# Optimization experiments

Hardware: AMD Instinct MI355X
Metric: run time of the kernel (lower is better)

Reference implementation:

```python
import math
import jax, jax.numpy as jnp
import numpy as np

B, N, TOKEN_DIM = 8, 8192, 512
NODE_DIM = 64
MAX_NODES = 64
SCORE_HIDDEN = 64


def setup_inputs() -> dict:
    key = jax.random.key(0)
    ks = jax.random.split(key, 8)
    s = lambda k, shape, fan_in: jax.random.normal(k, shape, jnp.float32) / np.sqrt(fan_in)
    return {
        "token_feats": jax.random.normal(ks[0], (B, N, TOKEN_DIM), jnp.float32),
        "score_w1": s(ks[1], (TOKEN_DIM, SCORE_HIDDEN), TOKEN_DIM),
        "score_b1": jnp.zeros((SCORE_HIDDEN,), jnp.float32),
        "score_w2": s(ks[2], (SCORE_HIDDEN, 1), SCORE_HIDDEN),
        "score_b2": jnp.zeros((1,), jnp.float32),
        "t2n_w": s(ks[3], (TOKEN_DIM, NODE_DIM), TOKEN_DIM),
        "n2t_w": s(ks[4], (NODE_DIM, TOKEN_DIM), NODE_DIM),
        "gcn_w1": s(ks[5], (NODE_DIM, NODE_DIM), NODE_DIM),
        "gcn_w2": s(ks[6], (NODE_DIM, NODE_DIM), NODE_DIM),
    }


def reference(token_feats, score_w1, score_b1, score_w2, score_b2,
              t2n_w, n2t_w, gcn_w1, gcn_w2):
    Bn, Nn, d = token_feats.shape
    M = MAX_NODES
    eps = 1e-6

    # --- node selection (scores -> threshold -> top-k among selected) ---
    h = jax.nn.relu(jnp.einsum('bnd,dh->bnh', token_feats, score_w1) + score_b1)
    scores = (jnp.einsum('bnh,ho->bno', h, score_w2) + score_b2)[..., 0]  # [B,N]
    mean = scores.mean(axis=1, keepdims=True)
    std = scores.std(axis=1, keepdims=True)  # unbiased=False (population)
    thr = mean + 0.5 * std
    count = jnp.sum(scores > thr, axis=1)  # [B]
    fallback_k = min(M, max(4, Nn // 16))
    take_k = jnp.where(count == 0, fallback_k, jnp.minimum(count, M))  # [B]

    _, top_idx = jax.lax.top_k(scores, M)  # [B,M] highest scores; set == torch's selection
    node_mask = jnp.arange(M)[None, :] < take_k[:, None]  # [B,M] bool
    maskf = node_mask.astype(token_feats.dtype)

    gathered = jnp.take_along_axis(token_feats, top_idx[..., None], axis=1)  # [B,M,d]
    H0 = jnp.einsum('bmd,dk->bmk', gathered, t2n_w) * maskf[..., None]  # [B,M,node_dim]

    # --- cosine-similarity adjacency, masked, self-loops, row-normalized ---
    nrm = jnp.maximum(jnp.linalg.norm(H0, axis=-1, keepdims=True), eps)
    Hn = H0 / nrm
    A = jax.nn.relu(jnp.einsum('bik,bjk->bij', Hn, Hn))
    A = A * (maskf[:, :, None] * maskf[:, None, :])
    A = A + jnp.eye(M, dtype=A.dtype)[None] * maskf[:, None, :]
    A = A / jnp.maximum(A.sum(axis=-1, keepdims=True), 1e-6)

    # --- two-layer GCN (no bias) ---
    x = jax.nn.relu(jnp.einsum('bij,bjk,kl->bil', A, H0, gcn_w1))
    Hg = jax.nn.relu(jnp.einsum('bij,bjk,kl->bil', A, x, gcn_w2))  # [B,M,node_dim]

    # --- attention scatter-back to tokens ---
    token_proj = jnp.einsum('bnd,dk->bnk', token_feats, t2n_w)  # [B,N,node_dim]
    logits = jnp.einsum('bnk,bmk->bnm', token_proj, Hg) / math.sqrt(NODE_DIM)
    attn = jax.nn.softmax(logits, axis=-1)
    injected = jnp.einsum('bnm,bmk->bnk', attn, Hg)
    back = jnp.einsum('bnk,kd->bnd', injected, n2t_w)
    return token_feats + back
```

## Files before the change

### kernel.cpp

```cpp
#include <hip/hip_runtime.h>
#include <hip/hip_bf16.h>

#define B_ 8
#define N_ 8192
#define D_ 512
#define M_ 64

typedef unsigned short u16;
typedef unsigned int u32;
typedef __attribute__((ext_vector_type(8))) short bf16x8;
typedef __attribute__((ext_vector_type(4))) float f32x4;

__device__ __forceinline__ u16 f2bf(float f) {
  u32 u = __float_as_uint(f);
  u += 0x7FFFu + ((u >> 16) & 1u);
  return (u16)(u >> 16);
}
__device__ __forceinline__ float bf2f(u16 h) {
  return __uint_as_float(((u32)h) << 16);
}

__device__ __forceinline__ int bfrag_idx(int kd, int c, int ncols16) {
  int sub = (kd >> 5) * ncols16 + (c >> 4);
  int lane = (c & 15) + 16 * ((kd & 15) >> 2);
  int e = (kd & 3) + 4 * ((kd >> 4) & 1);
  return sub * 512 + lane * 8 + e;
}

__device__ __forceinline__ int kslot(int ln, int e) {
  return (e & 3) + 4 * (ln >> 4) + 16 * (e >> 2);
}

__device__ __forceinline__ bf16x8 pack8(float4 v0, float4 v1) {
  bf16x8 a;
  a[0] = (short)f2bf(v0.x); a[1] = (short)f2bf(v0.y);
  a[2] = (short)f2bf(v0.z); a[3] = (short)f2bf(v0.w);
  a[4] = (short)f2bf(v1.x); a[5] = (short)f2bf(v1.y);
  a[6] = (short)f2bf(v1.z); a[7] = (short)f2bf(v1.w);
  return a;
}

__global__ __launch_bounds__(256) void k_prep(
    const float* __restrict__ t2n, const float* __restrict__ n2t,
    const float* __restrict__ W1, const float* __restrict__ g1,
    const float* __restrict__ g2,
    u16* __restrict__ t2nf, u16* __restrict__ n2tf,
    u16* __restrict__ W1h, u16* __restrict__ W1l,
    u16* __restrict__ g1f, u16* __restrict__ g2f)
{
  const int gid = blockIdx.x * 256 + threadIdx.x;
  const int stride = gridDim.x * 256;
  for (int s = gid; s < 512 * 64; s += stride) {
    const int k = s >> 6, c = s & 63;
    const int idx = bfrag_idx(k, c, 4);
    t2nf[idx] = f2bf(t2n[s]);
    const float w = W1[s];
    const u16 wh = f2bf(w);
    W1h[idx] = wh;
    W1l[idx] = f2bf(w - bf2f(wh));
  }
  for (int s = gid; s < 64 * 512; s += stride) {
    const int k = s >> 9, c = s & 511;
    n2tf[bfrag_idx(k, c, 32)] = f2bf(n2t[s]);
  }
  for (int s = gid; s < 4096; s += stride) {
    const int k = s >> 6, c = s & 63;
    g1f[bfrag_idx(k, c, 4)] = f2bf(g1[s]);
    g2f[bfrag_idx(k, c, 4)] = f2bf(g2[s]);
  }
}

__global__ __launch_bounds__(256, 4) void k_sp(
    const float* __restrict__ X, const u16* __restrict__ W1h,
    const u16* __restrict__ W1l, const u16* __restrict__ t2nf,
    const float* __restrict__ b1, const float* __restrict__ w2,
    const float* __restrict__ b2, float* __restrict__ scores,
    float* __restrict__ outStash)
{
  __shared__ __align__(16) u16 sB[6144];
  __shared__ __align__(16) u16 sAf[4096];
  const int tid = threadIdx.x;
  const int t0 = blockIdx.x * 64;
  const int wv = tid >> 6, ln = tid & 63;
  const int lq = ln >> 4, lr = ln & 15;
  u16* mySf = &sAf[wv * 1024];
  const float* xr = X + (size_t)(t0 + 16 * wv + lr) * D_;

  f32x4 acc[4], accP[4];
  #pragma unroll
  for (int cb = 0; cb < 4; ++cb) {
    acc[cb] = (f32x4){0.f, 0.f, 0.f, 0.f};
    accP[cb] = (f32x4){0.f, 0.f, 0.f, 0.f};
  }

  auto gsrc = [&](int f, int kb) -> const u16* {
    const int cb = f / 3, mat = f % 3;
    const u16* mp = (mat == 0) ? W1h : (mat == 1) ? W1l : t2nf;
    return mp + (kb * 4 + cb) * 512 + ln * 8;
  };

  bf16x8 wr[3];
  #pragma unroll
  for (int j = 0; j < 3; ++j) wr[j] = *(const bf16x8*)gsrc(j * 4 + wv, 0);
  float4 va0 = *(const float4*)(xr + 4 * lq);
  float4 va1 = *(const float4*)(xr + 16 + 4 * lq);

  for (int kb = 0; kb < 16; ++kb) {
    __syncthreads();
    #pragma unroll
    for (int j = 0; j < 3; ++j)
      *(bf16x8*)&sB[(j * 4 + wv) * 512 + ln * 8] = wr[j];
    __syncthreads();
    const float4 v0 = va0, v1 = va1;
    if (kb < 15) {
      #pragma unroll
      for (int j = 0; j < 3; ++j) wr[j] = *(const bf16x8*)gsrc(j * 4 + wv, kb + 1);
      va0 = *(const float4*)(xr + 32 * (kb + 1) + 4 * lq);
      va1 = *(const float4*)(xr + 32 * (kb + 1) + 16 + 4 * lq);
    }
    const float xs[8] = {v0.x, v0.y, v0.z, v0.w, v1.x, v1.y, v1.z, v1.w};
    bf16x8 ah, al;
    #pragma unroll
    for (int e = 0; e < 8; ++e) {
      const u16 h = f2bf(xs[e]);
      ah[e] = (short)h;
      al[e] = (short)f2bf(xs[e] - bf2f(h));
    }
    #pragma unroll
    for (int cb = 0; cb < 4; ++cb) {
      const bf16x8 bh = *(const bf16x8*)&sB[(cb * 3 + 0) * 512 + ln * 8];
      const bf16x8 bl = *(const bf16x8*)&sB[(cb * 3 + 1) * 512 + ln * 8];
      const bf16x8 bt = *(const bf16x8*)&sB[(cb * 3 + 2) * 512 + ln * 8];
      acc[cb]  = __builtin_amdgcn_mfma_f32_16x16x32_bf16(ah, bh, acc[cb], 0, 0, 0);
      acc[cb]  = __builtin_amdgcn_mfma_f32_16x16x32_bf16(ah, bl, acc[cb], 0, 0, 0);
      acc[cb]  = __builtin_amdgcn_mfma_f32_16x16x32_bf16(al, bh, acc[cb], 0, 0, 0);
      accP[cb] = __builtin_amdgcn_mfma_f32_16x16x32_bf16(ah, bt, accP[cb], 0, 0, 0);
    }
  }

  float b1v[4], w2v[4];
  #pragma unroll
  for (int cb = 0; cb < 4; ++cb) {
    const int col = cb * 16 + lr;
    b1v[cb] = b1[col]; w2v[cb] = w2[col];
  }
  const float b2v = b2[0];
  #pragma unroll
  for (int r = 0; r < 4; ++r) {
    float p = 0.f;
    #pragma unroll
    for (int cb = 0; cb < 4; ++cb) {
      const float h = fmaxf(acc[cb][r] + b1v[cb], 0.f);
      p = fmaf(h, w2v[cb], p);
    }
    p += __shfl_xor(p, 1); p += __shfl_xor(p, 2);
    p += __shfl_xor(p, 4); p += __shfl_xor(p, 8);
    if (lr == 0) scores[t0 + wv * 16 + 4 * lq + r] = p + b2v;
  }

  #pragma unroll
  for (int cb = 0; cb < 4; ++cb)
    #pragma unroll
    for (int r = 0; r < 4; ++r) {
      const int idx = (cb >> 1) * 512 + (4 * lq + r + 16 * (lr >> 2)) * 8 +
                      (lr & 3) + 4 * (cb & 1);
      mySf[idx] = f2bf(accP[cb][r]);
    }
  u16* stash = (u16*)(outStash + (size_t)blockIdx.x * 32768);
  #pragma unroll
  for (int kb2 = 0; kb2 < 2; ++kb2)
    *(bf16x8*)&stash[wv * 1024 + kb2 * 512 + ln * 8] =
        *(const bf16x8*)&mySf[kb2 * 512 + ln * 8];
}

__global__ __launch_bounds__(1024) void k_select(
    const float* __restrict__ scores, int* __restrict__ top_idx,
    int* __restrict__ take_k)
{
  __shared__ float sS[N_];
  __shared__ u32 hist[256];
  __shared__ float redf[34];
  __shared__ u32 redu[16];
  __shared__ u32 sPrefix, sRank, sCntA, sCntT;
  __shared__ int candIdx[64];
  __shared__ float candVal[64];
  __shared__ int tieIdx[128];
  const int b = blockIdx.x, tid = threadIdx.x;
  const int wv = tid >> 6, ln = tid & 63;
  const float* s = scores + (size_t)b * N_;

  float sum = 0.f, sq = 0.f;
  for (int i = tid; i < N_; i += 1024) {
    const float v = s[i]; sS[i] = v; sum += v; sq = fmaf(v, v, sq);
  }
  #pragma unroll
  for (int off = 32; off > 0; off >>= 1) {
    sum += __shfl_xor(sum, off);
    sq  += __shfl_xor(sq, off);
  }
  if (ln == 0) { redf[wv] = sum; redf[16 + wv] = sq; }
  __syncthreads();
  if (tid == 0) {
    float tot = 0.f, totq = 0.f;
    #pragma unroll
    for (int w = 0; w < 16; ++w) { tot += redf[w]; totq += redf[16 + w]; }
    const float mean = tot / (float)N_;
    const float var  = totq / (float)N_ - mean * mean;
    redf[32] = mean + 0.5f * sqrtf(fmaxf(var, 0.f));
  }
  __syncthreads();
  const float thr = redf[32];
  int c = 0;
  for (int i = tid; i < N_; i += 1024) c += (sS[i] > thr) ? 1 : 0;
  #pragma unroll
  for (int off = 32; off > 0; off >>= 1) c += __shfl_xor(c, off);
  if (ln == 0) redu[wv] = (u32)c;
  __syncthreads();
  if (tid == 0) {
    int cnt = 0;
    #pragma unroll
    for (int w = 0; w < 16; ++w) cnt += (int)redu[w];
    take_k[b] = (cnt == 0) ? M_ : (cnt < M_ ? cnt : M_);
  }
  __syncthreads();

  u32 prefix = 0, rank = 64, pmask = 0;
  for (int pass = 0; pass < 4; ++pass) {
    const int shift = 24 - 8 * pass;
    if (tid < 256) hist[tid] = 0;
    __syncthreads();
    for (int i = tid; i < N_; i += 1024) {
      const u32 u = __float_as_uint(sS[i]);
      const u32 key = u ^ ((u32)((int)u >> 31) | 0x80000000u);
      const bool active = (key & pmask) == prefix;
      const int bin = (int)((key >> shift) & 255u);
      if (pass == 0) {
        unsigned long long act = __ballot(active);
        while (act) {
          const int leader = (int)__builtin_ctzll(act);
          const int lbin = __shfl(bin, leader);
          const unsigned long long eq = __ballot(active && (bin == lbin));
          if (ln == leader) atomicAdd(&hist[lbin], (u32)__builtin_popcountll(eq));
          act &= ~eq;
        }
      } else {
        if (active) atomicAdd(&hist[bin], 1u);
      }
    }
    __syncthreads();
    if (tid < 64) {
      const u32 h0 = hist[4 * tid], h1 = hist[4 * tid + 1];
      const u32 h2 = hist[4 * tid + 2], h3 = hist[4 * tid + 3];
      const u32 s3 = h3, s2 = h2 + s3, s1 = h1 + s2, s0 = h0 + s1;
      u32 run = s0;
      #pragma unroll
      for (int off = 1; off < 64; off <<= 1) {
        const u32 t = (u32)__shfl_down((int)run, off);
        if (tid + off < 64) run += t;
      }
      const u32 excl = run - s0;
      const u32 c0 = s0 + excl, c1 = s1 + excl, c2 = s2 + excl, c3 = s3 + excl;
      int pick = -1; u32 nxt = 0;
      if (c0 >= rank && c1 < rank)        { pick = 0; nxt = c1; }
      else if (c1 >= rank && c2 < rank)   { pick = 1; nxt = c2; }
      else if (c2 >= rank && c3 < rank)   { pick = 2; nxt = c3; }
      else if (c3 >= rank && excl < rank) { pick = 3; nxt = excl; }
      if (pick >= 0) {
        sPrefix = prefix | ((u32)(4 * tid + pick) << shift);
        sRank = rank - nxt;
      }
    }
    __syncthreads();
    prefix = sPrefix; rank = sRank;
    pmask |= 0xFFu << shift;
    __syncthreads();
  }

  if (tid == 0) { sCntA = 0; sCntT = 0; }
  __syncthreads();
  const u32 pivot = prefix;
  for (int i = tid; i < N_; i += 1024) {
    const u32 u = __float_as_uint(sS[i]);
    const u32 key = u ^ ((u32)((int)u >> 31) | 0x80000000u);
    if (key > pivot) {
      const u32 p = atomicAdd(&sCntA, 1u);
      candIdx[p] = i; candVal[p] = sS[i];
    } else if (key == pivot) {
      const u32 p = atomicAdd(&sCntT, 1u);
      if (p < 128) tieIdx[p] = i;
    }
  }
  __syncthreads();
  if (tid == 0) {
    const int nA = (int)sCntA;
    const int need = 64 - nA;
    int nT = (int)sCntT; if (nT > 128) nT = 128;
    for (int j = 0; j < need; ++j) {
      int bi = 1 << 30, bp = -1;
      for (int q = 0; q < nT; ++q) {
        const int v = tieIdx[q];
        if (v >= 0 && v < bi) { bi = v; bp = q; }
      }
      candIdx[nA + j] = bi; candVal[nA + j] = sS[bi]; tieIdx[bp] = -1;
    }
  }
  __syncthreads();
  if (tid < 64) {
    const float v = candVal[tid]; const int ii = candIdx[tid];
    int rk = 0;
    for (int j = 0; j < 64; ++j) {
      const float vj = candVal[j]; const int ij = candIdx[j];
      rk += (vj > v || (vj == v && ij < ii)) ? 1 : 0;
    }
    top_idx[b * M_ + rk] = ii;
  }
}

__device__ __forceinline__ bf16x8 ldsA_frag(const float (*S)[65], int wv, int kb, int ln) {
  const int lr = ln & 15;
  bf16x8 a;
  #pragma unroll
  for (int e = 0; e < 8; ++e) a[e] = (short)f2bf(S[16 * wv + lr][32 * kb + kslot(ln, e)]);
  return a;
}
__device__ __forceinline__ bf16x8 ldsB_frag(const float (*S)[65], int cb, int kb, int ln) {
  const int lr = ln & 15;
  bf16x8 bb;
  #pragma unroll
  for (int e = 0; e < 8; ++e) bb[e] = (short)f2bf(S[32 * kb + kslot(ln, e)][16 * cb + lr]);
  return bb;
}
__device__ __forceinline__ bf16x8 ldsBT_frag(const float (*S)[65], int cb, int kb, int ln) {
  const int lr = ln & 15;
  bf16x8 bb;
  #pragma unroll
  for (int e = 0; e < 8; ++e) bb[e] = (short)f2bf(S[16 * cb + lr][32 * kb + kslot(ln, e)]);
  return bb;
}

__global__ __launch_bounds__(256) void k_graph(
    const float* __restrict__ X, const u16* __restrict__ t2nf,
    const u16* __restrict__ n2tf, const u16* __restrict__ g1f,
    const u16* __restrict__ g2f, const int* __restrict__ top_idx,
    const int* __restrict__ take_k, u16* __restrict__ HgTf,
    u16* __restrict__ Wf)
{
  __shared__ float sH0[64][65];
  __shared__ float sA[64][65];
  __shared__ float sT[64][65];
  __shared__ float sU[64][65];
  __shared__ float sR[64];
  const int b = blockIdx.x, tid = threadIdx.x;
  const int wv = tid >> 6, ln = tid & 63;
  const int lq = ln >> 4, lr = ln & 15;
  const int tk = take_k[b];
  const int rowm = 16 * wv + 4 * lq;

  const int gidx = top_idx[b * M_ + 16 * wv + lr];
  const float* xr = X + ((size_t)b * N_ + gidx) * D_;
  f32x4 d[4];
  #pragma unroll
  for (int cb = 0; cb < 4; ++cb) d[cb] = (f32x4){0.f, 0.f, 0.f, 0.f};
  {
    float4 p0[3], p1[3];
    #pragma unroll
    for (int q = 0; q < 3; ++q) {
      p0[q] = *(const float4*)(xr + 32 * q + 4 * lq);
      p1[q] = *(const float4*)(xr + 32 * q + 16 + 4 * lq);
    }
    #pragma unroll
    for (int kb = 0; kb < 16; ++kb) {
      const int slot = kb % 3;
      const float4 v0 = p0[slot], v1 = p1[slot];
      if (kb + 3 < 16) {
        p0[slot] = *(const float4*)(xr + 32 * (kb + 3) + 4 * lq);
        p1[slot] = *(const float4*)(xr + 32 * (kb + 3) + 16 + 4 * lq);
      }
      const bf16x8 a = pack8(v0, v1);
      #pragma unroll
      for (int cb = 0; cb < 4; ++cb) {
        const bf16x8 bb = *(const bf16x8*)&t2nf[(kb * 4 + cb) * 512 + ln * 8];
        d[cb] = __builtin_amdgcn_mfma_f32_16x16x32_bf16(a, bb, d[cb], 0, 0, 0);
      }
    }
  }
  #pragma unroll
  for (int cb = 0; cb < 4; ++cb)
    #pragma unroll
    for (int r = 0; r < 4; ++r)
      sH0[rowm + r][16 * cb + lr] = (rowm + r < tk) ? d[cb][r] : 0.f;
  __syncthreads();

  if (tid < 64) {
    float s = 0.f;
    #pragma unroll
    for (int k = 0; k < 64; ++k) { const float v = sH0[tid][k]; s = fmaf(v, v, s); }
    sR[tid] = 1.f / fmaxf(sqrtf(s), 1e-6f);
  }
  __syncthreads();
  #pragma unroll
  for (int p = 0; p < 16; ++p) {
    const int o = tid + p * 256;
    const int i = o >> 6, k = o & 63;
    sU[i][k] = sH0[i][k] * sR[i];
  }
  __syncthreads();

  #pragma unroll
  for (int cb = 0; cb < 4; ++cb) d[cb] = (f32x4){0.f, 0.f, 0.f, 0.f};
  #pragma unroll
  for (int kb = 0; kb < 2; ++kb) {
    const bf16x8 a = ldsA_frag(sU, wv, kb, ln);
    #pragma unroll
    for (int cb = 0; cb < 4; ++cb)
      d[cb] = __builtin_amdgcn_mfma_f32_16x16x32_bf16(a, ldsBT_frag(sU, cb, kb, ln), d[cb], 0, 0, 0);
  }
  __syncthreads();
  #pragma unroll
  for (int cb = 0; cb < 4; ++cb)
    #pragma unroll
    for (int r = 0; r < 4; ++r) {
      const int row = rowm + r, col = 16 * cb + lr;
      float s = fmaxf(d[cb][r], 0.f);
      s = (row < tk && col < tk) ? s : 0.f;
      if (row == col && row < tk) s += 1.f;
      sA[row][col] = s;
    }
  __syncthreads();

  if (tid < 64) {
    float rs = 0.f;
    #pragma unroll
    for (int j = 0; j < 64; ++j) rs += sA[tid][j];
    sR[tid] = 1.f / fmaxf(rs, 1e-6f);
  }
  __syncthreads();
  #pragma unroll
  for (int p = 0; p < 16; ++p) {
    const int o = tid + p * 256;
    const int i = o >> 6, j = o & 63;
    sA[i][j] *= sR[i];
  }
  __syncthreads();

  #pragma unroll
  for (int cb = 0; cb < 4; ++cb) d[cb] = (f32x4){0.f, 0.f, 0.f, 0.f};
  #pragma unroll
  for (int kb = 0; kb < 2; ++kb) {
    const bf16x8 a = ldsA_frag(sA, wv, kb, ln);
    #pragma unroll
    for (int cb = 0; cb < 4; ++cb)
      d[cb] = __builtin_amdgcn_mfma_f32_16x16x32_bf16(a, ldsB_frag(sH0, cb, kb, ln), d[cb], 0, 0, 0);
  }
  __syncthreads();
  #pragma unroll
  for (int cb = 0; cb < 4; ++cb)
    #pragma unroll
    for (int r = 0; r < 4; ++r) sT[rowm + r][16 * cb + lr] = d[cb][r];
  __syncthreads();

  #pragma unroll
  for (int cb = 0; cb < 4; ++cb) d[cb] = (f32x4){0.f, 0.f, 0.f, 0.f};
  #pragma unroll
  for (int kb = 0; kb < 2; ++kb) {
    const bf16x8 a = ldsA_frag(sT, wv, kb, ln);
    #pragma unroll
    for (int cb = 0; cb < 4; ++cb) {
      const bf16x8 bb = *(const bf16x8*)&g1f[(kb * 4 + cb) * 512 + ln * 8];
      d[cb] = __builtin_amdgcn_mfma_f32_16x16x32_bf16(a, bb, d[cb], 0, 0, 0);
    }
  }
  __syncthreads();
  #pragma unroll
  for (int cb = 0; cb < 4; ++cb)
    #pragma unroll
    for (int r = 0; r < 4; ++r) sU[rowm + r][16 * cb + lr] = fmaxf(d[cb][r], 0.f);
  __syncthreads();

  #pragma unroll
  for (int cb = 0; cb < 4; ++cb) d[cb] = (f32x4){0.f, 0.f, 0.f, 0.f};
  #pragma unroll
  for (int kb = 0; kb < 2; ++kb) {
    const bf16x8 a = ldsA_frag(sA, wv, kb, ln);
    #pragma unroll
    for (int cb = 0; cb < 4; ++cb)
      d[cb] = __builtin_amdgcn_mfma_f32_16x16x32_bf16(a, ldsB_frag(sU, cb, kb, ln), d[cb], 0, 0, 0);
  }
  __syncthreads();
  #pragma unroll
  for (int cb = 0; cb < 4; ++cb)
    #pragma unroll
    for (int r = 0; r < 4; ++r) sT[rowm + r][16 * cb + lr] = d[cb][r];
  __syncthreads();

  #pragma unroll
  for (int cb = 0; cb < 4; ++cb) d[cb] = (f32x4){0.f, 0.f, 0.f, 0.f};
  #pragma unroll
  for (int kb = 0; kb < 2; ++kb) {
    const bf16x8 a = ldsA_frag(sT, wv, kb, ln);
    #pragma unroll
    for (int cb = 0; cb < 4; ++cb) {
      const bf16x8 bb = *(const bf16x8*)&g2f[(kb * 4 + cb) * 512 + ln * 8];
      d[cb] = __builtin_amdgcn_mfma_f32_16x16x32_bf16(a, bb, d[cb], 0, 0, 0);
    }
  }
  __syncthreads();
  #pragma unroll
  for (int cb = 0; cb < 4; ++cb)
    #pragma unroll
    for (int r = 0; r < 4; ++r) {
      const int node = rowm + r, feat = 16 * cb + lr;
      const float hv = fmaxf(d[cb][r], 0.f);
      HgTf[(size_t)b * 4096 + bfrag_idx(feat, node, 4)] = f2bf(hv);
      sU[node][feat] = hv;
    }
  __syncthreads();

  for (int chk = 0; chk < 4; ++chk) {
    f32x4 aw[8];
    #pragma unroll
    for (int c8 = 0; c8 < 8; ++c8) aw[c8] = (f32x4){0.f, 0.f, 0.f, 0.f};
    #pragma unroll
    for (int kbf = 0; kbf < 2; ++kbf) {
      const bf16x8 a = ldsA_frag(sU, wv, kbf, ln);
      #pragma unroll
      for (int c8 = 0; c8 < 8; ++c8) {
        const bf16x8 bb = *(const bf16x8*)&n2tf[(kbf * 32 + chk * 8 + c8) * 512 + ln * 8];
        aw[c8] = __builtin_amdgcn_mfma_f32_16x16x32_bf16(a, bb, aw[c8], 0, 0, 0);
      }
    }
    #pragma unroll
    for (int c8 = 0; c8 < 8; ++c8)
      #pragma unroll
      for (int r = 0; r < 4; ++r) {
        const int m = 16 * wv + 4 * lq + r;
        const int c = (chk * 8 + c8) * 16 + lr;
        Wf[(size_t)b * 32768 + bfrag_idx(m, c, 32)] = f2bf(aw[c8][r]);
      }
  }
}

__global__ __launch_bounds__(256) void k_attn(
    const float* __restrict__ X, const u16* __restrict__ HgTf,
    const u16* __restrict__ Wf, float* __restrict__ out)
{
  __shared__ __align__(16) u16 sAf[4096];
  __shared__ __align__(16) float sBo[4][16][68];
  const int tid = threadIdx.x;
  const int b = blockIdx.x >> 7;
  const int t0 = (blockIdx.x & 127) << 6;
  const float* Xb = X + (size_t)b * N_ * D_;
  float* Ob = out + (size_t)b * N_ * D_;
  const int wv = tid >> 6, ln = tid & 63;
  const int lq = ln >> 4, lr = ln & 15;
  u16* mySf = &sAf[wv * 1024];
  const u16* stash = (const u16*)(out + (size_t)blockIdx.x * 32768);

  f32x4 accL[4];
  #pragma unroll
  for (int cb = 0; cb < 4; ++cb) accL[cb] = (f32x4){0.f, 0.f, 0.f, 0.f};
  #pragma unroll
  for (int kb = 0; kb < 2; ++kb) {
    const bf16x8 a = *(const bf16x8*)&stash[wv * 1024 + kb * 512 + ln * 8];
    #pragma unroll
    for (int cb = 0; cb < 4; ++cb) {
      const bf16x8 bb = *(const bf16x8*)&HgTf[(size_t)b * 4096 + (kb * 4 + cb) * 512 + ln * 8];
      accL[cb] = __builtin_amdgcn_mfma_f32_16x16x32_bf16(a, bb, accL[cb], 0, 0, 0);
    }
  }
  __syncthreads();

  float attnv[4][4];
  #pragma unroll
  for (int r = 0; r < 4; ++r) {
    const float v0 = accL[0][r], v1 = accL[1][r], v2 = accL[2][r], v3 = accL[3][r];
    float mx = fmaxf(fmaxf(v0, v1), fmaxf(v2, v3));
    mx = fmaxf(mx, __shfl_xor(mx, 1)); mx = fmaxf(mx, __shfl_xor(mx, 2));
    mx = fmaxf(mx, __shfl_xor(mx, 4)); mx = fmaxf(mx, __shfl_xor(mx, 8));
    const float e0 = __expf((v0 - mx) * 0.125f), e1 = __expf((v1 - mx) * 0.125f);
    const float e2 = __expf((v2 - mx) * 0.125f), e3 = __expf((v3 - mx) * 0.125f);
    float sm = (e0 + e1) + (e2 + e3);
    sm += __shfl_xor(sm, 1); sm += __shfl_xor(sm, 2);
    sm += __shfl_xor(sm, 4); sm += __shfl_xor(sm, 8);
    const float inv = 1.f / sm;
    attnv[0][r] = e0 * inv; attnv[1][r] = e1 * inv;
    attnv[2][r] = e2 * inv; attnv[3][r] = e3 * inv;
  }
  #pragma unroll
  for (int cb = 0; cb < 4; ++cb)
    #pragma unroll
    for (int r = 0; r < 4; ++r) {
      const int idx = (cb >> 1) * 512 + (4 * lq + r + 16 * (lr >> 2)) * 8 +
                      (lr & 3) + 4 * (cb & 1);
      mySf[idx] = f2bf(attnv[cb][r]);
    }

  for (int chk = 0; chk < 4; ++chk) {
    float4 xres[8];
    #pragma unroll
    for (int h = 0; h < 2; ++h)
      #pragma unroll
      for (int j = 0; j < 4; ++j)
        xres[h * 4 + j] = *(const float4*)(
            Xb + (size_t)(t0 + 16 * wv + 4 * j + lq) * D_ + chk * 128 + h * 64 + 4 * lr);

    f32x4 accB[8];
    #pragma unroll
    for (int c8 = 0; c8 < 8; ++c8) accB[c8] = (f32x4){0.f, 0.f, 0.f, 0.f};
    #pragma unroll
    for (int kb = 0; kb < 2; ++kb) {
      const bf16x8 a = *(const bf16x8*)&mySf[kb * 512 + ln * 8];
      #pragma unroll
      for (int c8 = 0; c8 < 8; ++c8) {
        const bf16x8 bb = *(const bf16x8*)&Wf[(size_t)b * 32768 + (kb * 32 + chk * 8 + c8) * 512 + ln * 8];
        accB[c8] = __builtin_amdgcn_mfma_f32_16x16x32_bf16(a, bb, accB[c8], 0, 0, 0);
      }
    }
    #pragma unroll
    for (int h = 0; h < 2; ++h) {
      #pragma unroll
      for (int c4 = 0; c4 < 4; ++c4)
        #pragma unroll
        for (int r = 0; r < 4; ++r)
          sBo[wv][4 * lq + r][c4 * 16 + lr] = accB[4 * h + c4][r];
      #pragma unroll
      for (int j = 0; j < 4; ++j) {
        const int rloc = 4 * j + lq;
        float4 v = *(const float4*)&sBo[wv][rloc][4 * lr];
        const float4 xv = xres[h * 4 + j];
        v.x += xv.x; v.y += xv.y; v.z += xv.z; v.w += xv.w;
        *(float4*)(Ob + (size_t)(t0 + 16 * wv + rloc) * D_ + chk * 128 + h * 64 + 4 * lr) = v;
      }
    }
  }
}

extern "C" void kernel_launch(void* const* d_in, const int* in_sizes, int n_in,
                              void* d_out, int out_size, void* d_ws, size_t ws_size,
                              hipStream_t stream)
{
  (void)in_sizes; (void)n_in; (void)out_size; (void)ws_size;
  const float* X   = (const float*)d_in[0];
  const float* W1  = (const float*)d_in[1];
  const float* b1  = (const float*)d_in[2];
  const float* w2  = (const float*)d_in[3];
  const float* b2  = (const float*)d_in[4];
  const float* t2n = (const float*)d_in[5];
  const float* n2t = (const float*)d_in[6];
  const float* g1  = (const float*)d_in[7];
  const float* g2  = (const float*)d_in[8];
  float* out = (float*)d_out;

  char* ws = (char*)d_ws;
  float* scores = (float*)(ws);
  u16* t2nf     = (u16*)(ws + 262144);
  u16* n2tf     = (u16*)(ws + 327680);
  u16* W1h      = (u16*)(ws + 393216);
  u16* W1l      = (u16*)(ws + 458752);
  u16* HgTf     = (u16*)(ws + 524288);
  u16* g1f      = (u16*)(ws + 589824);
  u16* g2f      = (u16*)(ws + 598016);
  int* top_idx  = (int*)(ws + 606208);
  int* take_k   = (int*)(ws + 608256);
  u16* Wf       = (u16*)(ws + 609280);

  k_prep<<<64, 256, 0, stream>>>(t2n, n2t, W1, g1, g2, t2nf, n2tf, W1h, W1l, g1f, g2f);
  k_sp<<<1024, 256, 0, stream>>>(X, W1h, W1l, t2nf, b1, w2, b2, scores, out);
  k_select<<<B_, 1024, 0, stream>>>(scores, top_idx, take_k);
  k_graph<<<B_, 256, 0, stream>>>(X, t2nf, n2tf, g1f, g2f, top_idx, take_k, HgTf, Wf);
  k_attn<<<1024, 256, 0, stream>>>(X, HgTf, Wf, out);
}
```

Before: 132.3 us.

## Fuse selection and graph kernels; double-buffer weight tiles in scoring kernel

Merges the per-batch top-k selection kernel and the GCN graph kernel into one 1024-thread kernel, so top indices and take_k stay in shared memory and one launch is removed. The first radix histogram pass is folded into the threshold-count loop to save a pass over the scores. In the scoring kernel the weight tile in LDS is double-buffered, which cuts one barrier per k-step. The fused kernel leaves 768 threads idle during the GCN matmuls, and its larger LDS footprint raises resource use.

```diff
diff --git a/kernel.cpp b/kernel.cpp
--- a/kernel.cpp
+++ b/kernel.cpp
@@ -77,7 +77,7 @@
     const float* __restrict__ b2, float* __restrict__ scores,
     float* __restrict__ outStash)
 {
-  __shared__ __align__(16) u16 sB[6144];
+  __shared__ __align__(16) u16 sB[2][6144];
   __shared__ __align__(16) u16 sAf[4096];
   const int tid = threadIdx.x;
   const int t0 = blockIdx.x * 64;
@@ -101,20 +101,27 @@
 
   bf16x8 wr[3];
   #pragma unroll
-  for (int j = 0; j < 3; ++j) wr[j] = *(const bf16x8*)gsrc(j * 4 + wv, 0);
+  for (int j = 0; j < 3; ++j)
+    *(bf16x8*)&sB[0][(j * 4 + wv) * 512 + ln * 8] = *(const bf16x8*)gsrc(j * 4 + wv, 0);
+  #pragma unroll
+  for (int j = 0; j < 3; ++j) wr[j] = *(const bf16x8*)gsrc(j * 4 + wv, 1);
   float4 va0 = *(const float4*)(xr + 4 * lq);
   float4 va1 = *(const float4*)(xr + 16 + 4 * lq);
+  __syncthreads();
 
   for (int kb = 0; kb < 16; ++kb) {
-    __syncthreads();
-    #pragma unroll
-    for (int j = 0; j < 3; ++j)
-      *(bf16x8*)&sB[(j * 4 + wv) * 512 + ln * 8] = wr[j];
-    __syncthreads();
+    const int cur = kb & 1;
+    if (kb < 15) {
+      #pragma unroll
+      for (int j = 0; j < 3; ++j)
+        *(bf16x8*)&sB[cur ^ 1][(j * 4 + wv) * 512 + ln * 8] = wr[j];
+    }
+    if (kb < 14) {
+      #pragma unroll
+      for (int j = 0; j < 3; ++j) wr[j] = *(const bf16x8*)gsrc(j * 4 + wv, kb + 2);
+    }
     const float4 v0 = va0, v1 = va1;
     if (kb < 15) {
-      #pragma unroll
-      for (int j = 0; j < 3; ++j) wr[j] = *(const bf16x8*)gsrc(j * 4 + wv, kb + 1);
       va0 = *(const float4*)(xr + 32 * (kb + 1) + 4 * lq);
       va1 = *(const float4*)(xr + 32 * (kb + 1) + 16 + 4 * lq);
     }
@@ -128,14 +135,15 @@
     }
     #pragma unroll
     for (int cb = 0; cb < 4; ++cb) {
-      const bf16x8 bh = *(const bf16x8*)&sB[(cb * 3 + 0) * 512 + ln * 8];
-      const bf16x8 bl = *(const bf16x8*)&sB[(cb * 3 + 1) * 512 + ln * 8];
-      const bf16x8 bt = *(const bf16x8*)&sB[(cb * 3 + 2) * 512 + ln * 8];
+      const bf16x8 bh = *(const bf16x8*)&sB[cur][(cb * 3 + 0) * 512 + ln * 8];
+      const bf16x8 bl = *(const bf16x8*)&sB[cur][(cb * 3 + 1) * 512 + ln * 8];
+      const bf16x8 bt = *(const bf16x8*)&sB[cur][(cb * 3 + 2) * 512 + ln * 8];
       acc[cb]  = __builtin_amdgcn_mfma_f32_16x16x32_bf16(ah, bh, acc[cb], 0, 0, 0);
       acc[cb]  = __builtin_amdgcn_mfma_f32_16x16x32_bf16(ah, bl, acc[cb], 0, 0, 0);
       acc[cb]  = __builtin_amdgcn_mfma_f32_16x16x32_bf16(al, bh, acc[cb], 0, 0, 0);
       accP[cb] = __builtin_amdgcn_mfma_f32_16x16x32_bf16(ah, bt, accP[cb], 0, 0, 0);
     }
+    __syncthreads();
   }
 
   float b1v[4], w2v[4];
@@ -173,9 +181,33 @@
         *(const bf16x8*)&mySf[kb2 * 512 + ln * 8];
 }
 
-__global__ __launch_bounds__(1024) void k_select(
-    const float* __restrict__ scores, int* __restrict__ top_idx,
-    int* __restrict__ take_k)
+__device__ __forceinline__ bf16x8 ldsA_frag(const float (*S)[65], int wv, int kb, int ln) {
+  const int lr = ln & 15;
+  bf16x8 a;
+  #pragma unroll
+  for (int e = 0; e < 8; ++e) a[e] = (short)f2bf(S[16 * wv + lr][32 * kb + kslot(ln, e)]);
+  return a;
+}
+__device__ __forceinline__ bf16x8 ldsB_frag(const float (*S)[65], int cb, int kb, int ln) {
+  const int lr = ln & 15;
+  bf16x8 bb;
+  #pragma unroll
+  for (int e = 0; e < 8; ++e) bb[e] = (short)f2bf(S[32 * kb + kslot(ln, e)][16 * cb + lr]);
+  return bb;
+}
+__device__ __forceinline__ bf16x8 ldsBT_frag(const float (*S)[65], int cb, int kb, int ln) {
+  const int lr = ln & 15;
+  bf16x8 bb;
+  #pragma unroll
+  for (int e = 0; e < 8; ++e) bb[e] = (short)f2bf(S[16 * cb + lr][32 * kb + kslot(ln, e)]);
+  return bb;
+}
+
+__global__ __launch_bounds__(1024) void k_selgraph(
+    const float* __restrict__ scores, const float* __restrict__ X,
+    const u16* __restrict__ t2nf, const u16* __restrict__ n2tf,
+    const u16* __restrict__ g1f, const u16* __restrict__ g2f,
+    u16* __restrict__ HgTf, u16* __restrict__ Wf)
 {
   __shared__ float sS[N_];
   __shared__ u32 hist[256];
@@ -185,14 +217,24 @@
   __shared__ int candIdx[64];
   __shared__ float candVal[64];
   __shared__ int tieIdx[128];
+  __shared__ int sTop[64];
+  __shared__ int sTk;
+  __shared__ float sH0[64][65];
+  __shared__ float sA[64][65];
+  __shared__ float sT[64][65];
+  __shared__ float sU[64][65];
+  __shared__ float sR[64];
+
   const int b = blockIdx.x, tid = threadIdx.x;
   const int wv = tid >> 6, ln = tid & 63;
+  const int lq = ln >> 4, lr = ln & 15;
   const float* s = scores + (size_t)b * N_;
 
   float sum = 0.f, sq = 0.f;
   for (int i = tid; i < N_; i += 1024) {
     const float v = s[i]; sS[i] = v; sum += v; sq = fmaf(v, v, sq);
   }
+  if (tid < 256) hist[tid] = 0;
   #pragma unroll
   for (int off = 32; off > 0; off >>= 1) {
     sum += __shfl_xor(sum, off);
@@ -211,7 +253,21 @@
   __syncthreads();
   const float thr = redf[32];
   int c = 0;
-  for (int i = tid; i < N_; i += 1024) c += (sS[i] > thr) ? 1 : 0;
+  for (int i = tid; i < N_; i += 1024) {
+    const float v = sS[i];
+    c += (v > thr) ? 1 : 0;
+    const u32 u = __float_as_uint(v);
+    const u32 key = u ^ ((u32)((int)u >> 31) | 0x80000000u);
+    const int bin = (int)(key >> 24);
+    unsigned long long act = ~0ull;
+    while (act) {
+      const int leader = (int)__builtin_ctzll(act);
+      const int lbin = __shfl(bin, leader);
+      const unsigned long long eq = __ballot(bin == lbin);
+      if (ln == leader) atomicAdd(&hist[lbin], (u32)__builtin_popcountll(eq));
+      act &= ~eq;
+    }
+  }
   #pragma unroll
   for (int off = 32; off > 0; off >>= 1) c += __shfl_xor(c, off);
   if (ln == 0) redu[wv] = (u32)c;
@@ -220,31 +276,19 @@
     int cnt = 0;
     #pragma unroll
     for (int w = 0; w < 16; ++w) cnt += (int)redu[w];
-    take_k[b] = (cnt == 0) ? M_ : (cnt < M_ ? cnt : M_);
-  }
-  __syncthreads();
+    sTk = (cnt == 0) ? M_ : (cnt < M_ ? cnt : M_);
+  }
 
   u32 prefix = 0, rank = 64, pmask = 0;
   for (int pass = 0; pass < 4; ++pass) {
     const int shift = 24 - 8 * pass;
-    if (tid < 256) hist[tid] = 0;
-    __syncthreads();
-    for (int i = tid; i < N_; i += 1024) {
-      const u32 u = __float_as_uint(sS[i]);
-      const u32 key = u ^ ((u32)((int)u >> 31) | 0x80000000u);
-      const bool active = (key & pmask) == prefix;
-      const int bin = (int)((key >> shift) & 255u);
-      if (pass == 0) {
-        unsigned long long act = __ballot(active);
-        while (act) {
-          const int leader = (int)__builtin_ctzll(act);
-          const int lbin = __shfl(bin, leader);
-          const unsigned long long eq = __ballot(active && (bin == lbin));
-          if (ln == leader) atomicAdd(&hist[lbin], (u32)__builtin_popcountll(eq));
-          act &= ~eq;
-        }
-      } else {
-        if (active) atomicAdd(&hist[bin], 1u);
+    if (pass > 0) {
+      if (tid < 256) hist[tid] = 0;
+      __syncthreads();
+      for (int i = tid; i < N_; i += 1024) {
+        const u32 u = __float_as_uint(sS[i]);
+        const u32 key = u ^ ((u32)((int)u >> 31) | 0x80000000u);
+        if ((key & pmask) == prefix) atomicAdd(&hist[(key >> shift) & 255u], 1u);
       }
     }
     __syncthreads();
@@ -312,56 +356,19 @@
       const float vj = candVal[j]; const int ij = candIdx[j];
       rk += (vj > v || (vj == v && ij < ii)) ? 1 : 0;
     }
-    top_idx[b * M_ + rk] = ii;
-  }
-}
-
-__device__ __forceinline__ bf16x8 ldsA_frag(const float (*S)[65], int wv, int kb, int ln) {
-  const int lr = ln & 15;
-  bf16x8 a;
-  #pragma unroll
-  for (int e = 0; e < 8; ++e) a[e] = (short)f2bf(S[16 * wv + lr][32 * kb + kslot(ln, e)]);
-  return a;
-}
-__device__ __forceinline__ bf16x8 ldsB_frag(const float (*S)[65], int cb, int kb, int ln) {
-  const int lr = ln & 15;
-  bf16x8 bb;
-  #pragma unroll
-  for (int e = 0; e < 8; ++e) bb[e] = (short)f2bf(S[32 * kb + kslot(ln, e)][16 * cb + lr]);
-  return bb;
-}
-__device__ __forceinline__ bf16x8 ldsBT_frag(const float (*S)[65], int cb, int kb, int ln) {
-  const int lr = ln & 15;
-  bf16x8 bb;
-  #pragma unroll
-  for (int e = 0; e < 8; ++e) bb[e] = (short)f2bf(S[16 * cb + lr][32 * kb + kslot(ln, e)]);
-  return bb;
-}
-
-__global__ __launch_bounds__(256) void k_graph(
-    const float* __restrict__ X, const u16* __restrict__ t2nf,
-    const u16* __restrict__ n2tf, const u16* __restrict__ g1f,
-    const u16* __restrict__ g2f, const int* __restrict__ top_idx,
-    const int* __restrict__ take_k, u16* __restrict__ HgTf,
-    u16* __restrict__ Wf)
-{
-  __shared__ float sH0[64][65];
-  __shared__ float sA[64][65];
-  __shared__ float sT[64][65];
-  __shared__ float sU[64][65];
-  __shared__ float sR[64];
-  const int b = blockIdx.x, tid = threadIdx.x;
-  const int wv = tid >> 6, ln = tid & 63;
-  const int lq = ln >> 4, lr = ln & 15;
-  const int tk = take_k[b];
+    sTop[rk] = ii;
+  }
+  __syncthreads();
+
+  const int tk = sTk;
   const int rowm = 16 * wv + 4 * lq;
-
-  const int gidx = top_idx[b * M_ + 16 * wv + lr];
-  const float* xr = X + ((size_t)b * N_ + gidx) * D_;
   f32x4 d[4];
-  #pragma unroll
-  for (int cb = 0; cb < 4; ++cb) d[cb] = (f32x4){0.f, 0.f, 0.f, 0.f};
-  {
+
+  if (tid < 256) {
+    const int gidx = sTop[16 * wv + lr];
+    const float* xr = X + ((size_t)b * N_ + gidx) * D_;
+    #pragma unroll
+    for (int cb = 0; cb < 4; ++cb) d[cb] = (f32x4){0.f, 0.f, 0.f, 0.f};
     float4 p0[3], p1[3];
     #pragma unroll
     for (int q = 0; q < 3; ++q) {
@@ -383,49 +390,52 @@
         d[cb] = __builtin_amdgcn_mfma_f32_16x16x32_bf16(a, bb, d[cb], 0, 0, 0);
       }
     }
-  }
-  #pragma unroll
-  for (int cb = 0; cb < 4; ++cb)
-    #pragma unroll
-    for (int r = 0; r < 4; ++r)
-      sH0[rowm + r][16 * cb + lr] = (rowm + r < tk) ? d[cb][r] : 0.f;
+    #pragma unroll
+    for (int cb = 0; cb < 4; ++cb)
+      #pragma unroll
+      for (int r = 0; r < 4; ++r)
+        sH0[rowm + r][16 * cb + lr] = (rowm + r < tk) ? d[cb][r] : 0.f;
+  }
   __syncthreads();
 
   if (tid < 64) {
-    float s = 0.f;
-    #pragma unroll
-    for (int k = 0; k < 64; ++k) { const float v = sH0[tid][k]; s = fmaf(v, v, s); }
-    sR[tid] = 1.f / fmaxf(sqrtf(s), 1e-6f);
-  }
-  __syncthreads();
-  #pragma unroll
-  for (int p = 0; p < 16; ++p) {
-    const int o = tid + p * 256;
-    const int i = o >> 6, k = o & 63;
-    sU[i][k] = sH0[i][k] * sR[i];
-  }
-  __syncthreads();
-
-  #pragma unroll
-  for (int cb = 0; cb < 4; ++cb) d[cb] = (f32x4){0.f, 0.f, 0.f, 0.f};
-  #pragma unroll
-  for (int kb = 0; kb < 2; ++kb) {
-    const bf16x8 a = ldsA_frag(sU, wv, kb, ln);
+    float ss = 0.f;
+    #pragma unroll
+    for (int k = 0; k < 64; ++k) { const float v = sH0[tid][k]; ss = fmaf(v, v, ss); }
+    sR[tid] = 1.f / fmaxf(sqrtf(ss), 1e-6f);
+  }
+  __syncthreads();
+  #pragma unroll
+  for (int p = 0; p < 4; ++p) {
+    const int o = tid + p * 1024;
+    sU[o >> 6][o & 63] = sH0[o >> 6][o & 63] * sR[o >> 6];
+  }
+  __syncthreads();
+
+  if (tid < 256) {
+    #pragma unroll
+    for (int cb = 0; cb < 4; ++cb) d[cb] = (f32x4){0.f, 0.f, 0.f, 0.f};
+    #pragma unroll
+    for (int kb = 0; kb < 2; ++kb) {
+      const bf16x8 a = ldsA_frag(sU, wv, kb, ln);
+      #pragma unroll
+      for (int cb = 0; cb < 4; ++cb)
+        d[cb] = __builtin_amdgcn_mfma_f32_16x16x32_bf16(a, ldsBT_frag(sU, cb, kb, ln), d[cb], 0, 0, 0);
+    }
+  }
+  __syncthreads();
+  if (tid < 256) {
     #pragma unroll
     for (int cb = 0; cb < 4; ++cb)
-      d[cb] = __builtin_amdgcn_mfma_f32_16x16x32_bf16(a, ldsBT_frag(sU, cb, kb, ln), d[cb], 0, 0, 0);
-  }
-  __syncthreads();
-  #pragma unroll
-  for (int cb = 0; cb < 4; ++cb)
-    #pragma unroll
-    for (int r = 0; r < 4; ++r) {
-      const int row = rowm + r, col = 16 * cb + lr;
-      float s = fmaxf(d[cb][r], 0.f);
-      s = (row < tk && col < tk) ? s : 0.f;
-      if (row == col && row < tk) s += 1.f;
-      sA[row][col] = s;
-    }
+      #pragma unroll
+      for (int r = 0; r < 4; ++r) {
+        const int row = rowm + r, col = 16 * cb + lr;
+        float v = fmaxf(d[cb][r], 0.f);
+        v = (row < tk && col < tk) ? v : 0.f;
+        if (row == col && row < tk) v += 1.f;
+        sA[row][col] = v;
+      }
+  }
   __syncthreads();
 
   if (tid < 64) {
@@ -436,107 +446,124 @@
   }
   __syncthreads();
   #pragma unroll
-  for (int p = 0; p < 16; ++p) {
-    const int o = tid + p * 256;
-    const int i = o >> 6, j = o & 63;
-    sA[i][j] *= sR[i];
-  }
-  __syncthreads();
-
-  #pragma unroll
-  for (int cb = 0; cb < 4; ++cb) d[cb] = (f32x4){0.f, 0.f, 0.f, 0.f};
-  #pragma unroll
-  for (int kb = 0; kb < 2; ++kb) {
-    const bf16x8 a = ldsA_frag(sA, wv, kb, ln);
+  for (int p = 0; p < 4; ++p) {
+    const int o = tid + p * 1024;
+    sA[o >> 6][o & 63] *= sR[o >> 6];
+  }
+  __syncthreads();
+
+  if (tid < 256) {
+    #pragma unroll
+    for (int cb = 0; cb < 4; ++cb) d[cb] = (f32x4){0.f, 0.f, 0.f, 0.f};
+    #pragma unroll
+    for (int kb = 0; kb < 2; ++kb) {
+      const bf16x8 a = ldsA_frag(sA, wv, kb, ln);
+      #pragma unroll
+      for (int cb = 0; cb < 4; ++cb)
+        d[cb] = __builtin_amdgcn_mfma_f32_16x16x32_bf16(a, ldsB_frag(sH0, cb, kb, ln), d[cb], 0, 0, 0);
+    }
+  }
+  __syncthreads();
+  if (tid < 256) {
     #pragma unroll
     for (int cb = 0; cb < 4; ++cb)
-      d[cb] = __builtin_amdgcn_mfma_f32_16x16x32_bf16(a, ldsB_frag(sH0, cb, kb, ln), d[cb], 0, 0, 0);
-  }
-  __syncthreads();
-  #pragma unroll
-  for (int cb = 0; cb < 4; ++cb)
-    #pragma unroll
-    for (int r = 0; r < 4; ++r) sT[rowm + r][16 * cb + lr] = d[cb][r];
-  __syncthreads();
-
-  #pragma unroll
-  for (int cb = 0; cb < 4; ++cb) d[cb] = (f32x4){0.f, 0.f, 0.f, 0.f};
-  #pragma unroll
-  for (int kb = 0; kb < 2; ++kb) {
-    const bf16x8 a = ldsA_frag(sT, wv, kb, ln);
-    #pragma unroll
-    for (int cb = 0; cb < 4; ++cb) {
-      const bf16x8 bb = *(const bf16x8*)&g1f[(kb * 4 + cb) * 512 + ln * 8];
-      d[cb] = __builtin_amdgcn_mfma_f32_16x16x32_bf16(a, bb, d[cb], 0, 0, 0);
-    }
-  }
-  __syncthreads();
-  #pragma unroll
-  for (int cb = 0; cb < 4; ++cb)
-    #pragma unroll
-    for (int r = 0; r < 4; ++r) sU[rowm + r][16 * cb + lr] = fmaxf(d[cb][r], 0.f);
-  __syncthreads();
-
-  #pragma unroll
-  for (int cb = 0; cb < 4; ++cb) d[cb] = (f32x4){0.f, 0.f, 0.f, 0.f};
-  #pragma unroll
-  for (int kb = 0; kb < 2; ++kb) {
-    const bf16x8 a = ldsA_frag(sA, wv, kb, ln);
+      #pragma unroll
+      for (int r = 0; r < 4; ++r) sT[rowm + r][16 * cb + lr] = d[cb][r];
+  }
+  __syncthreads();
+
+  if (tid < 256) {
+    #pragma unroll
+    for (int cb = 0; cb < 4; ++cb) d[cb] = (f32x4){0.f, 0.f, 0.f, 0.f};
+    #pragma unroll
+    for (int kb = 0; kb < 2; ++kb) {
+      const bf16x8 a = ldsA_frag(sT, wv, kb, ln);
+      #pragma unroll
+      for (int cb = 0; cb < 4; ++cb) {
+        const bf16x8 bb = *(const bf16x8*)&g1f[(kb * 4 + cb) * 512 + ln * 8];
+        d[cb] = __builtin_amdgcn_mfma_f32_16x16x32_bf16(a, bb, d[cb], 0, 0, 0);
+      }
+    }
+  }
+  __syncthreads();
+  if (tid < 256) {
     #pragma unroll
     for (int cb = 0; cb < 4; ++cb)
-      d[cb] = __builtin_amdgcn_mfma_f32_16x16x32_bf16(a, ldsB_frag(sU, cb, kb, ln), d[cb], 0, 0, 0);
-  }
-  __syncthreads();
-  #pragma unroll
-  for (int cb = 0; cb < 4; ++cb)
-    #pragma unroll
-    for (int r = 0; r < 4; ++r) sT[rowm + r][16 * cb + lr] = d[cb][r];
-  __syncthreads();
-
-  #pragma unroll
-  for (int cb = 0; cb < 4; ++cb) d[cb] = (f32x4){0.f, 0.f, 0.f, 0.f};
-  #pragma unroll
-  for (int kb = 0; kb < 2; ++kb) {
-    const bf16x8 a = ldsA_frag(sT, wv, kb, ln);
-    #pragma unroll
-    for (int cb = 0; cb < 4; ++cb) {
-      const bf16x8 bb = *(const bf16x8*)&g2f[(kb * 4 + cb) * 512 + ln * 8];
-      d[cb] = __builtin_amdgcn_mfma_f32_16x16x32_bf16(a, bb, d[cb], 0, 0, 0);
-    }
-  }
-  __syncthreads();
-  #pragma unroll
-  for (int cb = 0; cb < 4; ++cb)
-    #pragma unroll
-    for (int r = 0; r < 4; ++r) {
-      const int node = rowm + r, feat = 16 * cb + lr;
-      const float hv = fmaxf(d[cb][r], 0.f);
-      HgTf[(size_t)b * 4096 + bfrag_idx(feat, node, 4)] = f2bf(hv);
-      sU[node][feat] = hv;
-    }
-  __syncthreads();
-
-  for (int chk = 0; chk < 4; ++chk) {
-    f32x4 aw[8];
-    #pragma unroll
-    for (int c8 = 0; c8 < 8; ++c8) aw[c8] = (f32x4){0.f, 0.f, 0.f, 0.f};
-    #pragma unroll
-    for (int kbf = 0; kbf < 2; ++kbf) {
-      const bf16x8 a = ldsA_frag(sU, wv, kbf, ln);
-      #pragma unroll
-      for (int c8 = 0; c8 < 8; ++c8) {
-        const bf16x8 bb = *(const bf16x8*)&n2tf[(kbf * 32 + chk * 8 + c8) * 512 + ln * 8];
-        aw[c8] = __builtin_amdgcn_mfma_f32_16x16x32_bf16(a, bb, aw[c8], 0, 0, 0);
-      }
-    }
-    #pragma unroll
-    for (int c8 = 0; c8 < 8; ++c8)
+      #pragma unroll
+      for (int r = 0; r < 4; ++r) sU[rowm + r][16 * cb + lr] = fmaxf(d[cb][r], 0.f);
+  }
+  __syncthreads();
+
+  if (tid < 256) {
+    #pragma unroll
+    for (int cb = 0; cb < 4; ++cb) d[cb] = (f32x4){0.f, 0.f, 0.f, 0.f};
+    #pragma unroll
+    for (int kb = 0; kb < 2; ++kb) {
+      const bf16x8 a = ldsA_frag(sA, wv, kb, ln);
+      #pragma unroll
+      for (int cb = 0; cb < 4; ++cb)
+        d[cb] = __builtin_amdgcn_mfma_f32_16x16x32_bf16(a, ldsB_frag(sU, cb, kb, ln), d[cb], 0, 0, 0);
+    }
+  }
+  __syncthreads();
+  if (tid < 256) {
+    #pragma unroll
+    for (int cb = 0; cb < 4; ++cb)
+      #pragma unroll
+      for (int r = 0; r < 4; ++r) sT[rowm + r][16 * cb + lr] = d[cb][r];
+  }
+  __syncthreads();
+
+  if (tid < 256) {
+    #pragma unroll
+    for (int cb = 0; cb < 4; ++cb) d[cb] = (f32x4){0.f, 0.f, 0.f, 0.f};
+    #pragma unroll
+    for (int kb = 0; kb < 2; ++kb) {
+      const bf16x8 a = ldsA_frag(sT, wv, kb, ln);
+      #pragma unroll
+      for (int cb = 0; cb < 4; ++cb) {
+        const bf16x8 bb = *(const bf16x8*)&g2f[(kb * 4 + cb) * 512 + ln * 8];
+        d[cb] = __builtin_amdgcn_mfma_f32_16x16x32_bf16(a, bb, d[cb], 0, 0, 0);
+      }
+    }
+  }
+  __syncthreads();
+  if (tid < 256) {
+    #pragma unroll
+    for (int cb = 0; cb < 4; ++cb)
       #pragma unroll
       for (int r = 0; r < 4; ++r) {
-        const int m = 16 * wv + 4 * lq + r;
-        const int c = (chk * 8 + c8) * 16 + lr;
-        Wf[(size_t)b * 32768 + bfrag_idx(m, c, 32)] = f2bf(aw[c8][r]);
-      }
+        const int node = rowm + r, feat = 16 * cb + lr;
+        const float hv = fmaxf(d[cb][r], 0.f);
+        HgTf[(size_t)b * 4096 + bfrag_idx(feat, node, 4)] = f2bf(hv);
+        sU[node][feat] = hv;
+      }
+  }
+  __syncthreads();
+
+  if (tid < 256) {
+    for (int chk = 0; chk < 4; ++chk) {
+      f32x4 aw[8];
+      #pragma unroll
+      for (int c8 = 0; c8 < 8; ++c8) aw[c8] = (f32x4){0.f, 0.f, 0.f, 0.f};
+      #pragma unroll
+      for (int kbf = 0; kbf < 2; ++kbf) {
+        const bf16x8 a = ldsA_frag(sU, wv, kbf, ln);
+        #pragma unroll
+        for (int c8 = 0; c8 < 8; ++c8) {
+          const bf16x8 bb = *(const bf16x8*)&n2tf[(kbf * 32 + chk * 8 + c8) * 512 + ln * 8];
+          aw[c8] = __builtin_amdgcn_mfma_f32_16x16x32_bf16(a, bb, aw[c8], 0, 0, 0);
+        }
+      }
+      #pragma unroll
+      for (int c8 = 0; c8 < 8; ++c8)
+        #pragma unroll
+        for (int r = 0; r < 4; ++r) {
+          const int m = 16 * wv + 4 * lq + r;
+          const int cc = (chk * 8 + c8) * 16 + lr;
+          Wf[(size_t)b * 32768 + bfrag_idx(m, cc, 32)] = f2bf(aw[c8][r]);
+        }
+    }
   }
 }
 
@@ -660,13 +687,10 @@
   u16* HgTf     = (u16*)(ws + 524288);
   u16* g1f      = (u16*)(ws + 589824);
   u16* g2f      = (u16*)(ws + 598016);
-  int* top_idx  = (int*)(ws + 606208);
-  int* take_k   = (int*)(ws + 608256);
   u16* Wf       = (u16*)(ws + 609280);
 
   k_prep<<<64, 256, 0, stream>>>(t2n, n2t, W1, g1, g2, t2nf, n2tf, W1h, W1l, g1f, g2f);
   k_sp<<<1024, 256, 0, stream>>>(X, W1h, W1l, t2nf, b1, w2, b2, scores, out);
-  k_select<<<B_, 1024, 0, stream>>>(scores, top_idx, take_k);
-  k_graph<<<B_, 256, 0, stream>>>(X, t2nf, n2tf, g1f, g2f, top_idx, take_k, HgTf, Wf);
+  k_selgraph<<<B_, 1024, 0, stream>>>(scores, X, t2nf, n2tf, g1f, g2f, HgTf, Wf);
   k_attn<<<1024, 256, 0, stream>>>(X, HgTf, Wf, out);
 }
```

Result: no change. 131.4 us (-0.7%).
